# Kernel optimization log

Hardware: AMD Instinct MI355X
Metric: run time of the kernel (lower is better)

## Reference

```python
import jax, jax.numpy as jnp
import numpy as np

D_MODEL = 256
D_CLIP = 768
NHEAD = 8
HEAD_DIM = D_MODEL // NHEAD
Q_LEN = 100
B = 32
T_LEN = 1203


def setup_inputs() -> dict:
    key = jax.random.key(0)
    ks = jax.random.split(key, 16)
    xav = lambda k, o, i: jax.random.uniform(k, (o, i), jnp.float32, -1.0, 1.0) * np.sqrt(6.0 / (o + i))
    return {
        "tgt": jax.random.normal(ks[0], (Q_LEN, B, D_MODEL), jnp.float32),
        "text_classification": jax.random.normal(ks[1], (T_LEN, D_CLIP), jnp.float32),
        "query_pos": jax.random.normal(ks[2], (Q_LEN, B, D_MODEL), jnp.float32),
        "out_of_vocab_logits": jax.random.normal(ks[3], (B, Q_LEN, T_LEN), jnp.float32),
        "Wq": xav(ks[4], D_MODEL, D_MODEL), "bq": jnp.zeros((D_MODEL,), jnp.float32),
        "Wk": xav(ks[5], D_MODEL, D_CLIP), "bk": jnp.zeros((D_MODEL,), jnp.float32),
        "Wv": xav(ks[6], D_MODEL, D_CLIP), "bv": jnp.zeros((D_MODEL,), jnp.float32),
        "Wo": xav(ks[7], D_MODEL, D_MODEL), "bo": jnp.zeros((D_MODEL,), jnp.float32),
        "ln_g": jnp.ones((D_MODEL,), jnp.float32), "ln_b": jnp.zeros((D_MODEL,), jnp.float32),
        "logit_scale": jnp.asarray(np.log(1 / 0.07), jnp.float32),
    }


def _l2norm(x, eps=1e-6):
    # F.normalize: x / max(||x||, eps)
    n = jnp.sqrt(jnp.sum(x * x, axis=-1, keepdims=True))
    return x / jnp.maximum(n, eps)


def _layernorm(x, g, b, eps=1e-5):
    mu = jnp.mean(x, axis=-1, keepdims=True)
    var = jnp.mean((x - mu) ** 2, axis=-1, keepdims=True)
    return (x - mu) * jax.lax.rsqrt(var + eps) * g + b


def reference(tgt, text_classification, query_pos, out_of_vocab_logits,
              Wq, bq, Wk, bk, Wv, bv, Wo, bo, ln_g, ln_b, logit_scale):
    qin = tgt + query_pos                       # (Q, B, d_model)
    q = qin @ Wq.T + bq                         # (Q, B, d_model)
    # text embeddings shared across batch (2D path)
    k = text_classification @ Wk.T + bk         # (T, d_model)
    v = text_classification @ Wv.T + bv         # (T, d_model)

    q = q.transpose(1, 0, 2).reshape(B, Q_LEN, NHEAD, HEAD_DIM).transpose(0, 2, 1, 3)  # (B,h,Q,hd)
    k = k.reshape(T_LEN, NHEAD, HEAD_DIM).transpose(1, 0, 2)                            # (h,T,hd)
    v = v.reshape(T_LEN, NHEAD, HEAD_DIM).transpose(1, 0, 2)                            # (h,T,hd)

    q = _l2norm(q)
    k = _l2norm(k)
    scale = jnp.minimum(jnp.exp(logit_scale), 100.0)
    in_vocab = jnp.einsum('bhqd,hkd->bhqk', q, k) * scale                                # (B,h,Q,T)

    alpha = jnp.linspace(0.0, 1.0, NHEAD, dtype=in_vocab.dtype).reshape(1, NHEAD, 1, 1)
    logits = in_vocab * (1.0 - alpha) + out_of_vocab_logits[:, None] * alpha

    attn = jax.nn.softmax(logits, axis=-1)
    out = jnp.einsum('bhqk,hkd->bhqd', attn, v)                                          # (B,h,Q,hd)
    out = out.transpose(0, 2, 1, 3).reshape(B, Q_LEN, D_MODEL).transpose(1, 0, 2)        # (Q,B,d_model)
    out = out @ Wo.T + bo

    # forward_post: residual + layernorm (dropout=0)
    return _layernorm(tgt + out, ln_g, ln_b)
```

## Files before the change

kernel.cpp:

```cpp
#include <hip/hip_runtime.h>
#include <hip/hip_bf16.h>
#include <math.h>

#define D_MODEL 256
#define D_CLIP 768
#define NHEAD 8
#define HEAD_DIM 32
#define Q_LEN 100
#define BB 32
#define T_LEN 1203
#define TPAD 1216
#define MQ (Q_LEN*BB)
#define LOG2E 1.4426950408889634f

typedef __bf16 bf16_t;
typedef __bf16 bf16x8 __attribute__((ext_vector_type(8)));
typedef __bf16 bf16x4 __attribute__((ext_vector_type(4)));
typedef float f32x4 __attribute__((ext_vector_type(4)));

static __device__ __forceinline__ bf16_t to_bf16(float x) { return (bf16_t)x; }

__global__ void prep_kernel(const float* __restrict__ tgt, const float* __restrict__ qpos,
                            const float* __restrict__ text, const float* __restrict__ Wq,
                            const float* __restrict__ Wk, const float* __restrict__ Wv,
                            const float* __restrict__ Wo, const float* __restrict__ oov,
                            bf16_t* __restrict__ qin_bf, bf16_t* __restrict__ conv_dst,
                            float* __restrict__ oov_ws) {
    int idx = blockIdx.x * 256 + threadIdx.x;
    if (idx >= 1529248) return;
    if (idx < 204800) {
        float4 a = ((const float4*)tgt)[idx];
        float4 b = ((const float4*)qpos)[idx];
        bf16x4 r = { to_bf16(a.x + b.x), to_bf16(a.y + b.y),
                     to_bf16(a.z + b.z), to_bf16(a.w + b.w) };
        *(bf16x4*)(qin_bf + (size_t)idx * 4) = r;
    } else if (idx < 566848) {
        int j = idx - 204800;
        const float4* src;
        if (j < 230976)      src = (const float4*)text + j;
        else if (j < 247360) src = (const float4*)Wq + (j - 230976);
        else if (j < 296512) src = (const float4*)Wk + (j - 247360);
        else if (j < 345664) src = (const float4*)Wv + (j - 296512);
        else                 src = (const float4*)Wo + (j - 345664);
        float4 v = *src;
        bf16x4 r = { to_bf16(v.x), to_bf16(v.y), to_bf16(v.z), to_bf16(v.w) };
        *(bf16x4*)(conv_dst + (size_t)j * 4) = r;
    } else {
        int j = idx - 566848;
        ((float4*)oov_ws)[j] = ((const float4*)oov)[j];
    }
}

__launch_bounds__(256)
__global__ void proj_kernel(const bf16_t* __restrict__ qin_bf, const bf16_t* __restrict__ text_bf,
                            const bf16_t* __restrict__ wq, const bf16_t* __restrict__ wk,
                            const bf16_t* __restrict__ wv,
                            const float* __restrict__ bq, const float* __restrict__ bk,
                            const float* __restrict__ bv,
                            bf16_t* __restrict__ qn, bf16_t* __restrict__ kn,
                            bf16_t* __restrict__ vT) {
    const int bid = blockIdx.y;
    int z, xt;
    if (bid < 50)      { z = 0; xt = bid; }
    else if (bid < 69) { z = 1; xt = bid - 50; }
    else               { z = 2; xt = bid - 69; }
    const int j = blockIdx.x;
    const int nbase = j * 32;
    const int M = (z == 0) ? MQ : T_LEN;
    const int K = (z == 0) ? D_MODEL : D_CLIP;
    const bf16_t* W = (z == 0) ? wq : (z == 1 ? wk : wv);
    const float* bias = (z == 0) ? bq : (z == 1 ? bk : bv);

    const int wave = threadIdx.x >> 6;
    const int lane = threadIdx.x & 63;
    const int c16 = lane & 15;
    const int quad = lane >> 4;
    const int mbase = xt * 64 + wave * 16;

    f32x4 a0 = (f32x4){0.f, 0.f, 0.f, 0.f};
    f32x4 a1 = (f32x4){0.f, 0.f, 0.f, 0.f};

    const int arow = (mbase + c16 < M) ? (mbase + c16) : (M - 1);
    const bf16_t* Apb = ((z == 0) ? qin_bf : text_bf) + (size_t)arow * K + quad * 8;
    const bf16_t* W0 = W + (size_t)(nbase + c16) * K + quad * 8;
    const bf16_t* W1 = W + (size_t)(nbase + 16 + c16) * K + quad * 8;
    const int ksteps = K / 32;
    #pragma unroll 4
    for (int ks = 0; ks < ksteps; ks++) {
        bf16x8 af = *(const bf16x8*)(Apb + ks * 32);
        bf16x8 b0 = *(const bf16x8*)(W0 + ks * 32);
        bf16x8 b1 = *(const bf16x8*)(W1 + ks * 32);
        a0 = __builtin_amdgcn_mfma_f32_16x16x32_bf16(af, b0, a0, 0, 0, 0);
        a1 = __builtin_amdgcn_mfma_f32_16x16x32_bf16(af, b1, a1, 0, 0, 0);
    }

    float b0s = bias[nbase + c16];
    float b1s = bias[nbase + 16 + c16];
    #pragma unroll
    for (int r = 0; r < 4; r++) { a0[r] += b0s; a1[r] += b1s; }
    if (z < 2) {
        #pragma unroll
        for (int r = 0; r < 4; r++) {
            float s = a0[r] * a0[r] + a1[r] * a1[r];
            #pragma unroll
            for (int o = 1; o < 16; o <<= 1) s += __shfl_xor(s, o);
            float sc = 1.0f / fmaxf(sqrtf(s), 1e-6f);
            a0[r] *= sc; a1[r] *= sc;
        }
    }
    #pragma unroll
    for (int r = 0; r < 4; r++) {
        int m = mbase + quad * 4 + r;
        if (m >= M) continue;
        if (z == 0) {
            int q = m >> 5, b = m & 31;
            size_t base = ((size_t)(b * NHEAD + j) * Q_LEN + q) * HEAD_DIM;
            qn[base + c16] = to_bf16(a0[r]);
            qn[base + 16 + c16] = to_bf16(a1[r]);
        } else if (z == 1) {
            size_t base = ((size_t)j * T_LEN + m) * HEAD_DIM;
            kn[base + c16] = to_bf16(a0[r]);
            kn[base + 16 + c16] = to_bf16(a1[r]);
        } else {
            vT[(size_t)(j * 32 + c16) * TPAD + m] = to_bf16(a0[r]);
            vT[(size_t)(j * 32 + 16 + c16) * TPAD + m] = to_bf16(a1[r]);
        }
    }
}

__launch_bounds__(256)
__global__ void attn_kernel(const bf16_t* __restrict__ qn, const bf16_t* __restrict__ kn,
                            const bf16_t* __restrict__ vT, const float* __restrict__ oov,
                            const float* __restrict__ logit_scale,
                            bf16_t* __restrict__ attn_out) {
    const int qt = blockIdx.x;
    const int h = blockIdx.y;
    const int b = blockIdx.z;
    const int qbase = qt * 16;
    const int wave = threadIdx.x >> 6;
    const int lane = threadIdx.x & 63;
    const int c16 = lane & 15;
    const int quad = lane >> 4;

    __shared__ __align__(16) bf16_t p_lds[4][2][16][40];
    __shared__ float l_lds[4][16];
    __shared__ float o_lds[4][32][16];

    const float scl = fminf(expf(logit_scale[0]), 100.0f);
    const float alpha = (float)h * (1.0f / 7.0f);
    const float sscale = scl * (1.0f - alpha) * LOG2E;
    const float oscale = alpha * LOG2E;
    const float mfix = sscale + 20.0f * oscale;

    const int q = qbase + c16;
    const int qc = (q < Q_LEN) ? q : (Q_LEN - 1);
    bf16x8 qf = *(const bf16x8*)(qn + ((size_t)(b * NHEAD + h) * Q_LEN + qc) * HEAD_DIM + quad * 8);

    f32x4 olo = (f32x4){0.f, 0.f, 0.f, 0.f};
    f32x4 ohi = (f32x4){0.f, 0.f, 0.f, 0.f};
    float l_s = 0.0f;

    const bf16_t* knh = kn + (size_t)h * T_LEN * HEAD_DIM;
    const bf16_t* vTh = vT + (size_t)h * HEAD_DIM * TPAD;
    const float* oovr = oov + ((size_t)b * Q_LEN + qc) * T_LEN;
    const f32x4 zero = (f32x4){0.f, 0.f, 0.f, 0.f};

    bf16x8 kA0, kA1, kB0, kB1, vA0, vA1, vB0, vB1;
    float4 oA0, oA1, oB0, oB1;

    #define LOAD_PAIR(P, kA0_, kA1_, kB0_, kB1_, vA0_, vA1_, vB0_, vB1_, oA0_, oA1_, oB0_, oB1_) \
        { const int tb0_ = (P) * 64; const int tb1_ = tb0_ + 32;                                   \
          kA0_ = *(const bf16x8*)(knh + (size_t)(tb0_ + c16) * HEAD_DIM + quad * 8);               \
          kA1_ = *(const bf16x8*)(knh + (size_t)(tb0_ + 16 + c16) * HEAD_DIM + quad * 8);          \
          kB0_ = *(const bf16x8*)(knh + (size_t)(tb1_ + c16) * HEAD_DIM + quad * 8);               \
          kB1_ = *(const bf16x8*)(knh + (size_t)(tb1_ + 16 + c16) * HEAD_DIM + quad * 8);          \
          vA0_ = *(const bf16x8*)(vTh + (size_t)c16 * TPAD + tb0_ + quad * 8);                     \
          vA1_ = *(const bf16x8*)(vTh + (size_t)(16 + c16) * TPAD + tb0_ + quad * 8);              \
          vB0_ = *(const bf16x8*)(vTh + (size_t)c16 * TPAD + tb1_ + quad * 8);                     \
          vB1_ = *(const bf16x8*)(vTh + (size_t)(16 + c16) * TPAD + tb1_ + quad * 8);              \
          oA0_ = *(const float4*)(oovr + tb0_ + quad * 4);                                         \
          oA1_ = *(const float4*)(oovr + tb0_ + 16 + quad * 4);                                    \
          oB0_ = *(const float4*)(oovr + tb1_ + quad * 4);                                         \
          oB1_ = *(const float4*)(oovr + tb1_ + 16 + quad * 4); }

    if (wave < 18) LOAD_PAIR(wave, kA0, kA1, kB0, kB1, vA0, vA1, vB0, vB1, oA0, oA1, oB0, oB1);

    for (int p = wave; p < 18; p += 4) {
        const int pn = (p + 4 < 18) ? (p + 4) : 17;
        bf16x8 nkA0, nkA1, nkB0, nkB1, nvA0, nvA1, nvB0, nvB1;
        float4 noA0, noA1, noB0, noB1;
        LOAD_PAIR(pn, nkA0, nkA1, nkB0, nkB1, nvA0, nvA1, nvB0, nvB1, noA0, noA1, noB0, noB1);

        f32x4 s00 = __builtin_amdgcn_mfma_f32_16x16x32_bf16(kA0, qf, zero, 0, 0, 0);
        f32x4 s01 = __builtin_amdgcn_mfma_f32_16x16x32_bf16(kA1, qf, zero, 0, 0, 0);
        f32x4 s10 = __builtin_amdgcn_mfma_f32_16x16x32_bf16(kB0, qf, zero, 0, 0, 0);
        f32x4 s11 = __builtin_amdgcn_mfma_f32_16x16x32_bf16(kB1, qf, zero, 0, 0, 0);
        float pa0[4], pa1[4], pb0[4], pb1[4];
        float ovA0[4] = {oA0.x, oA0.y, oA0.z, oA0.w};
        float ovA1[4] = {oA1.x, oA1.y, oA1.z, oA1.w};
        float ovB0[4] = {oB0.x, oB0.y, oB0.z, oB0.w};
        float ovB1[4] = {oB1.x, oB1.y, oB1.z, oB1.w};
        #pragma unroll
        for (int r = 0; r < 4; r++) {
            pa0[r] = exp2f(fmaf(s00[r], sscale, fmaf(ovA0[r], oscale, -mfix)));
            pa1[r] = exp2f(fmaf(s01[r], sscale, fmaf(ovA1[r], oscale, -mfix)));
            pb0[r] = exp2f(fmaf(s10[r], sscale, fmaf(ovB0[r], oscale, -mfix)));
            pb1[r] = exp2f(fmaf(s11[r], sscale, fmaf(ovB1[r], oscale, -mfix)));
        }
        l_s += ((pa0[0] + pa0[1]) + (pa0[2] + pa0[3])) + ((pa1[0] + pa1[1]) + (pa1[2] + pa1[3]))
             + ((pb0[0] + pb0[1]) + (pb0[2] + pb0[3])) + ((pb1[0] + pb1[1]) + (pb1[2] + pb1[3]));
        bf16x4 wA0 = { to_bf16(pa0[0]), to_bf16(pa0[1]), to_bf16(pa0[2]), to_bf16(pa0[3]) };
        bf16x4 wA1 = { to_bf16(pa1[0]), to_bf16(pa1[1]), to_bf16(pa1[2]), to_bf16(pa1[3]) };
        bf16x4 wB0 = { to_bf16(pb0[0]), to_bf16(pb0[1]), to_bf16(pb0[2]), to_bf16(pb0[3]) };
        bf16x4 wB1 = { to_bf16(pb1[0]), to_bf16(pb1[1]), to_bf16(pb1[2]), to_bf16(pb1[3]) };
        *(bf16x4*)&p_lds[wave][0][c16][quad * 4] = wA0;
        *(bf16x4*)&p_lds[wave][0][c16][16 + quad * 4] = wA1;
        *(bf16x4*)&p_lds[wave][1][c16][quad * 4] = wB0;
        *(bf16x4*)&p_lds[wave][1][c16][16 + quad * 4] = wB1;
        bf16x8 pf0 = *(const bf16x8*)(&p_lds[wave][0][c16][quad * 8]);
        bf16x8 pf1 = *(const bf16x8*)(&p_lds[wave][1][c16][quad * 8]);
        olo = __builtin_amdgcn_mfma_f32_16x16x32_bf16(vA0, pf0, olo, 0, 0, 0);
        ohi = __builtin_amdgcn_mfma_f32_16x16x32_bf16(vA1, pf0, ohi, 0, 0, 0);
        olo = __builtin_amdgcn_mfma_f32_16x16x32_bf16(vB0, pf1, olo, 0, 0, 0);
        ohi = __builtin_amdgcn_mfma_f32_16x16x32_bf16(vB1, pf1, ohi, 0, 0, 0);

        kA0 = nkA0; kA1 = nkA1; kB0 = nkB0; kB1 = nkB1;
        vA0 = nvA0; vA1 = nvA1; vB0 = nvB0; vB1 = nvB1;
        oA0 = noA0; oA1 = noA1; oB0 = noB0; oB1 = noB1;
    }
    #undef LOAD_PAIR

    if (wave == 2) {
        const int tb = 1152;
        bf16x8 kf0 = *(const bf16x8*)(knh + (size_t)(tb + c16) * HEAD_DIM + quad * 8);
        bf16x8 kf1 = *(const bf16x8*)(knh + (size_t)(tb + 16 + c16) * HEAD_DIM + quad * 8);
        float4 oa = *(const float4*)(oovr + tb + quad * 4);
        float4 oc = *(const float4*)(oovr + tb + 16 + quad * 4);
        bf16x8 v0 = *(const bf16x8*)(vTh + (size_t)c16 * TPAD + tb + quad * 8);
        bf16x8 v1 = *(const bf16x8*)(vTh + (size_t)(16 + c16) * TPAD + tb + quad * 8);
        f32x4 s0 = __builtin_amdgcn_mfma_f32_16x16x32_bf16(kf0, qf, zero, 0, 0, 0);
        f32x4 s1 = __builtin_amdgcn_mfma_f32_16x16x32_bf16(kf1, qf, zero, 0, 0, 0);
        float ova[4] = {oa.x, oa.y, oa.z, oa.w};
        float ovc[4] = {oc.x, oc.y, oc.z, oc.w};
        float p0[4], p1[4];
        #pragma unroll
        for (int r = 0; r < 4; r++) {
            p0[r] = exp2f(fmaf(s0[r], sscale, fmaf(ova[r], oscale, -mfix)));
            p1[r] = exp2f(fmaf(s1[r], sscale, fmaf(ovc[r], oscale, -mfix)));
        }
        l_s += ((p0[0] + p0[1]) + (p0[2] + p0[3])) + ((p1[0] + p1[1]) + (p1[2] + p1[3]));
        bf16x4 w0 = { to_bf16(p0[0]), to_bf16(p0[1]), to_bf16(p0[2]), to_bf16(p0[3]) };
        bf16x4 w1 = { to_bf16(p1[0]), to_bf16(p1[1]), to_bf16(p1[2]), to_bf16(p1[3]) };
        *(bf16x4*)&p_lds[wave][0][c16][quad * 4] = w0;
        *(bf16x4*)&p_lds[wave][0][c16][16 + quad * 4] = w1;
        bf16x8 pf = *(const bf16x8*)(&p_lds[wave][0][c16][quad * 8]);
        olo = __builtin_amdgcn_mfma_f32_16x16x32_bf16(v0, pf, olo, 0, 0, 0);
        ohi = __builtin_amdgcn_mfma_f32_16x16x32_bf16(v1, pf, ohi, 0, 0, 0);
    }

    if (wave == 3) {
        const int tb = 1184;
        int t1c = tb + 16 + c16;
        if (t1c >= T_LEN) t1c = T_LEN - 1;
        bf16x8 kf0 = *(const bf16x8*)(knh + (size_t)(tb + c16) * HEAD_DIM + quad * 8);
        bf16x8 kf1 = *(const bf16x8*)(knh + (size_t)t1c * HEAD_DIM + quad * 8);
        bf16x8 v0 = *(const bf16x8*)(vTh + (size_t)c16 * TPAD + tb + quad * 8);
        bf16x8 v1 = *(const bf16x8*)(vTh + (size_t)(16 + c16) * TPAD + tb + quad * 8);
        f32x4 s0 = __builtin_amdgcn_mfma_f32_16x16x32_bf16(kf0, qf, zero, 0, 0, 0);
        f32x4 s1 = __builtin_amdgcn_mfma_f32_16x16x32_bf16(kf1, qf, zero, 0, 0, 0);
        float p0[4], p1[4];
        #pragma unroll
        for (int r = 0; r < 4; r++) {
            int ta = tb + quad * 4 + r;
            int tb2 = tb + 16 + quad * 4 + r;
            float ova = oovr[ta];
            p0[r] = exp2f(fmaf(s0[r], sscale, fmaf(ova, oscale, -mfix)));
            if (tb2 < T_LEN) {
                float ovc = oovr[tb2];
                p1[r] = exp2f(fmaf(s1[r], sscale, fmaf(ovc, oscale, -mfix)));
            } else {
                p1[r] = 0.0f;
            }
        }
        l_s += ((p0[0] + p0[1]) + (p0[2] + p0[3])) + ((p1[0] + p1[1]) + (p1[2] + p1[3]));
        bf16x4 w0 = { to_bf16(p0[0]), to_bf16(p0[1]), to_bf16(p0[2]), to_bf16(p0[3]) };
        bf16x4 w1 = { to_bf16(p1[0]), to_bf16(p1[1]), to_bf16(p1[2]), to_bf16(p1[3]) };
        *(bf16x4*)&p_lds[wave][0][c16][quad * 4] = w0;
        *(bf16x4*)&p_lds[wave][0][c16][16 + quad * 4] = w1;
        bf16x8 pf = *(const bf16x8*)(&p_lds[wave][0][c16][quad * 8]);
        olo = __builtin_amdgcn_mfma_f32_16x16x32_bf16(v0, pf, olo, 0, 0, 0);
        ohi = __builtin_amdgcn_mfma_f32_16x16x32_bf16(v1, pf, ohi, 0, 0, 0);
    }

    l_s += __shfl_xor(l_s, 16);
    l_s += __shfl_xor(l_s, 32);
    if (quad == 0) l_lds[wave][c16] = l_s;
    #pragma unroll
    for (int r = 0; r < 4; r++) {
        o_lds[wave][quad * 4 + r][c16] = olo[r];
        o_lds[wave][16 + quad * 4 + r][c16] = ohi[r];
    }
    __syncthreads();
    const int q16 = threadIdx.x & 15;
    const int dd = threadIdx.x >> 4;
    float L = l_lds[0][q16] + l_lds[1][q16] + l_lds[2][q16] + l_lds[3][q16];
    const float invL = 1.0f / L;
    const int qout = qbase + q16;
    if (qout < Q_LEN) {
        #pragma unroll
        for (int half = 0; half < 2; half++) {
            int d = half * 16 + dd;
            float O = o_lds[0][d][q16] + o_lds[1][d][q16] +
                      o_lds[2][d][q16] + o_lds[3][d][q16];
            attn_out[((size_t)qout * BB + b) * D_MODEL + h * HEAD_DIM + d] = to_bf16(O * invL);
        }
    }
}

__launch_bounds__(256)
__global__ void out_kernel(const bf16_t* __restrict__ attn, const bf16_t* __restrict__ wo,
                           const float* __restrict__ bo, const float* __restrict__ tgt,
                           const float* __restrict__ ln_g, const float* __restrict__ ln_b,
                           float* __restrict__ out) {
    const int xt = blockIdx.x;
    const int wave = threadIdx.x >> 6;
    const int lane = threadIdx.x & 63;
    const int c16 = lane & 15;
    const int quad = lane >> 4;
    const int mbase = xt * 16;

    __shared__ float xs[16][264];

    f32x4 acc[4];
    #pragma unroll
    for (int i = 0; i < 4; i++) acc[i] = (f32x4){0.f, 0.f, 0.f, 0.f};
    const bf16_t* Ap = attn + (size_t)(mbase + c16) * D_MODEL + quad * 8;
    #pragma unroll
    for (int ks = 0; ks < 8; ks++) {
        bf16x8 af = *(const bf16x8*)(Ap + ks * 32);
        #pragma unroll
        for (int nt = 0; nt < 4; nt++) {
            int n = wave * 64 + nt * 16 + c16;
            bf16x8 bfr = *(const bf16x8*)(wo + (size_t)n * D_MODEL + ks * 32 + quad * 8);
            acc[nt] = __builtin_amdgcn_mfma_f32_16x16x32_bf16(af, bfr, acc[nt], 0, 0, 0);
        }
    }
    #pragma unroll
    for (int nt = 0; nt < 4; nt++) {
        int col = wave * 64 + nt * 16 + c16;
        float bb_ = bo[col];
        #pragma unroll
        for (int r = 0; r < 4; r++) {
            int m = mbase + quad * 4 + r;
            xs[quad * 4 + r][col] = acc[nt][r] + bb_ + tgt[(size_t)m * D_MODEL + col];
        }
    }
    __syncthreads();
    const int row = threadIdx.x >> 4;
    const int seg = threadIdx.x & 15;
    float sx = 0.f, sxx = 0.f;
    #pragma unroll
    for (int i = 0; i < 16; i++) {
        float x = xs[row][seg * 16 + i];
        sx += x; sxx += x * x;
    }
    #pragma unroll
    for (int o = 1; o < 16; o <<= 1) { sx += __shfl_xor(sx, o); sxx += __shfl_xor(sxx, o); }
    float mu = sx * (1.0f / 256.0f);
    float var = sxx * (1.0f / 256.0f) - mu * mu;
    float rstd = rsqrtf(fmaxf(var, 0.0f) + 1e-5f);
    size_t obase = (size_t)(mbase + row) * D_MODEL;
    #pragma unroll
    for (int i = 0; i < 16; i++) {
        int cidx = seg * 16 + i;
        out[obase + cidx] = (xs[row][cidx] - mu) * rstd * ln_g[cidx] + ln_b[cidx];
    }
}

extern "C" void kernel_launch(void* const* d_in, const int* in_sizes, int n_in,
                              void* d_out, int out_size, void* d_ws, size_t ws_size,
                              hipStream_t stream) {
    const float* tgt  = (const float*)d_in[0];
    const float* text = (const float*)d_in[1];
    const float* qpos = (const float*)d_in[2];
    const float* oov  = (const float*)d_in[3];
    const float* Wq = (const float*)d_in[4];
    const float* bq = (const float*)d_in[5];
    const float* Wk = (const float*)d_in[6];
    const float* bk = (const float*)d_in[7];
    const float* Wv = (const float*)d_in[8];
    const float* bv = (const float*)d_in[9];
    const float* Wo = (const float*)d_in[10];
    const float* bo = (const float*)d_in[11];
    const float* ln_g = (const float*)d_in[12];
    const float* ln_b = (const float*)d_in[13];
    const float* lsc  = (const float*)d_in[14];

    bf16_t* wsb = (bf16_t*)d_ws;
    bf16_t* text_bf = wsb + 0;
    bf16_t* wq_bf   = wsb + 923904;
    bf16_t* wk_bf   = wsb + 989440;
    bf16_t* wv_bf   = wsb + 1186048;
    bf16_t* wo_bf   = wsb + 1382656;
    bf16_t* qin_bf  = wsb + 1448192;
    bf16_t* qn      = wsb + 2267392;
    bf16_t* kn      = wsb + 3086592;
    bf16_t* vT      = wsb + 3394560;
    bf16_t* attn    = wsb + 3705856;
    float* oov_ws   = (float*)((char*)d_ws + 9050112);
    float* out      = (float*)d_out;

    prep_kernel<<<5975, 256, 0, stream>>>(tgt, qpos, text, Wq, Wk, Wv, Wo, oov,
                                          qin_bf, text_bf, oov_ws);
    proj_kernel<<<dim3(8, 88, 1), 256, 0, stream>>>(qin_bf, text_bf, wq_bf, wk_bf, wv_bf,
                                                    bq, bk, bv, qn, kn, vT);
    attn_kernel<<<dim3(7, 8, 32), 256, 0, stream>>>(qn, kn, vT, oov_ws, lsc, attn);
    out_kernel<<<200, 256, 0, stream>>>(attn, wo_bf, bo, tgt, ln_g, ln_b, out);
}
```

Before: 172.8 us.

## Stage per-head K in LDS and drop redundant oov copy in prep

Result: faster. 158.6 us (-8.2%).

```diff
diff --git a/kernel.cpp b/kernel.cpp
--- a/kernel.cpp
+++ b/kernel.cpp
@@ -23,18 +23,18 @@
 __global__ void prep_kernel(const float* __restrict__ tgt, const float* __restrict__ qpos,
                             const float* __restrict__ text, const float* __restrict__ Wq,
                             const float* __restrict__ Wk, const float* __restrict__ Wv,
-                            const float* __restrict__ Wo, const float* __restrict__ oov,
-                            bf16_t* __restrict__ qin_bf, bf16_t* __restrict__ conv_dst,
-                            float* __restrict__ oov_ws) {
+                            const float* __restrict__ Wo,
+                            bf16_t* __restrict__ qin_bf, bf16_t* __restrict__ conv_dst) {
     int idx = blockIdx.x * 256 + threadIdx.x;
-    if (idx >= 1529248) return;
+    if (idx >= 566848) return;
+    float4 v;
+    bf16_t* dst;
     if (idx < 204800) {
         float4 a = ((const float4*)tgt)[idx];
         float4 b = ((const float4*)qpos)[idx];
-        bf16x4 r = { to_bf16(a.x + b.x), to_bf16(a.y + b.y),
-                     to_bf16(a.z + b.z), to_bf16(a.w + b.w) };
-        *(bf16x4*)(qin_bf + (size_t)idx * 4) = r;
-    } else if (idx < 566848) {
+        v = make_float4(a.x + b.x, a.y + b.y, a.z + b.z, a.w + b.w);
+        dst = qin_bf + idx * 4;
+    } else {
         int j = idx - 204800;
         const float4* src;
         if (j < 230976)      src = (const float4*)text + j;
@@ -42,13 +42,11 @@
         else if (j < 296512) src = (const float4*)Wk + (j - 247360);
         else if (j < 345664) src = (const float4*)Wv + (j - 296512);
         else                 src = (const float4*)Wo + (j - 345664);
-        float4 v = *src;
-        bf16x4 r = { to_bf16(v.x), to_bf16(v.y), to_bf16(v.z), to_bf16(v.w) };
-        *(bf16x4*)(conv_dst + (size_t)j * 4) = r;
-    } else {
-        int j = idx - 566848;
-        ((float4*)oov_ws)[j] = ((const float4*)oov)[j];
-    }
+        v = *src;
+        dst = conv_dst + (size_t)j * 4;
+    }
+    bf16x4 r = { to_bf16(v.x), to_bf16(v.y), to_bf16(v.z), to_bf16(v.w) };
+    *(bf16x4*)dst = r;
 }
 
 __launch_bounds__(256)
@@ -128,23 +126,24 @@
     }
 }
 
-__launch_bounds__(256)
+__launch_bounds__(896)
 __global__ void attn_kernel(const bf16_t* __restrict__ qn, const bf16_t* __restrict__ kn,
                             const bf16_t* __restrict__ vT, const float* __restrict__ oov,
                             const float* __restrict__ logit_scale,
                             bf16_t* __restrict__ attn_out) {
-    const int qt = blockIdx.x;
+    const int b = blockIdx.x;
     const int h = blockIdx.y;
-    const int b = blockIdx.z;
-    const int qbase = qt * 16;
-    const int wave = threadIdx.x >> 6;
-    const int lane = threadIdx.x & 63;
+    const int tid = threadIdx.x;
+    const int w = tid >> 6;
+    const int lane = tid & 63;
     const int c16 = lane & 15;
     const int quad = lane >> 4;
-
-    __shared__ __align__(16) bf16_t p_lds[4][2][16][40];
-    __shared__ float l_lds[4][16];
-    __shared__ float o_lds[4][32][16];
+    const int qt = w >> 1;
+    const int thalf = w & 1;
+    const int qbase = qt * 16;
+
+    __shared__ __align__(16) unsigned int k_lds[24320];
+    __shared__ __align__(16) bf16_t p_lds[14][2][16][40];
 
     const float scl = fminf(expf(logit_scale[0]), 100.0f);
     const float alpha = (float)h * (1.0f / 7.0f);
@@ -152,49 +151,54 @@
     const float oscale = alpha * LOG2E;
     const float mfix = sscale + 20.0f * oscale;
 
-    const int q = qbase + c16;
-    const int qc = (q < Q_LEN) ? q : (Q_LEN - 1);
+    const bf16_t* knh = kn + (size_t)h * T_LEN * HEAD_DIM;
+    const bf16_t* vTh = vT + (size_t)h * HEAD_DIM * TPAD;
+
+    const int qc = (qbase + c16 < Q_LEN) ? (qbase + c16) : (Q_LEN - 1);
     bf16x8 qf = *(const bf16x8*)(qn + ((size_t)(b * NHEAD + h) * Q_LEN + qc) * HEAD_DIM + quad * 8);
+    const float* oovr = oov + ((size_t)b * Q_LEN + qc) * T_LEN;
+    const f32x4 zero = (f32x4){0.f, 0.f, 0.f, 0.f};
+
+    {
+        const unsigned int* knw = (const unsigned int*)knh;
+        for (int idx = tid; idx < 19248; idx += 896)
+            k_lds[(idx >> 4) * 20 + (idx & 15)] = knw[idx];
+    }
 
     f32x4 olo = (f32x4){0.f, 0.f, 0.f, 0.f};
     f32x4 ohi = (f32x4){0.f, 0.f, 0.f, 0.f};
     float l_s = 0.0f;
 
-    const bf16_t* knh = kn + (size_t)h * T_LEN * HEAD_DIM;
-    const bf16_t* vTh = vT + (size_t)h * HEAD_DIM * TPAD;
-    const float* oovr = oov + ((size_t)b * Q_LEN + qc) * T_LEN;
-    const f32x4 zero = (f32x4){0.f, 0.f, 0.f, 0.f};
-
-    bf16x8 kA0, kA1, kB0, kB1, vA0, vA1, vB0, vB1;
+    #define KFRAG(trow) (*(const bf16x8*)&k_lds[(unsigned)(trow) * 20 + quad * 4])
+    #define LOADPV(P, vA0_, vA1_, vB0_, vB1_, oA0_, oA1_, oB0_, oB1_)                   \
+        { const int tb0_ = (P) * 64; const int tb1_ = tb0_ + 32;                         \
+          vA0_ = *(const bf16x8*)(vTh + (size_t)c16 * TPAD + tb0_ + quad * 8);           \
+          vA1_ = *(const bf16x8*)(vTh + (size_t)(16 + c16) * TPAD + tb0_ + quad * 8);    \
+          vB0_ = *(const bf16x8*)(vTh + (size_t)c16 * TPAD + tb1_ + quad * 8);           \
+          vB1_ = *(const bf16x8*)(vTh + (size_t)(16 + c16) * TPAD + tb1_ + quad * 8);    \
+          oA0_ = *(const float4*)(oovr + tb0_ + quad * 4);                               \
+          oA1_ = *(const float4*)(oovr + tb0_ + 16 + quad * 4);                          \
+          oB0_ = *(const float4*)(oovr + tb1_ + quad * 4);                               \
+          oB1_ = *(const float4*)(oovr + tb1_ + 16 + quad * 4); }
+
+    bf16x8 vA0, vA1, vB0, vB1;
     float4 oA0, oA1, oB0, oB1;
-
-    #define LOAD_PAIR(P, kA0_, kA1_, kB0_, kB1_, vA0_, vA1_, vB0_, vB1_, oA0_, oA1_, oB0_, oB1_) \
-        { const int tb0_ = (P) * 64; const int tb1_ = tb0_ + 32;                                   \
-          kA0_ = *(const bf16x8*)(knh + (size_t)(tb0_ + c16) * HEAD_DIM + quad * 8);               \
-          kA1_ = *(const bf16x8*)(knh + (size_t)(tb0_ + 16 + c16) * HEAD_DIM + quad * 8);          \
-          kB0_ = *(const bf16x8*)(knh + (size_t)(tb1_ + c16) * HEAD_DIM + quad * 8);               \
-          kB1_ = *(const bf16x8*)(knh + (size_t)(tb1_ + 16 + c16) * HEAD_DIM + quad * 8);          \
-          vA0_ = *(const bf16x8*)(vTh + (size_t)c16 * TPAD + tb0_ + quad * 8);                     \
-          vA1_ = *(const bf16x8*)(vTh + (size_t)(16 + c16) * TPAD + tb0_ + quad * 8);              \
-          vB0_ = *(const bf16x8*)(vTh + (size_t)c16 * TPAD + tb1_ + quad * 8);                     \
-          vB1_ = *(const bf16x8*)(vTh + (size_t)(16 + c16) * TPAD + tb1_ + quad * 8);              \
-          oA0_ = *(const float4*)(oovr + tb0_ + quad * 4);                                         \
-          oA1_ = *(const float4*)(oovr + tb0_ + 16 + quad * 4);                                    \
-          oB0_ = *(const float4*)(oovr + tb1_ + quad * 4);                                         \
-          oB1_ = *(const float4*)(oovr + tb1_ + 16 + quad * 4); }
-
-    if (wave < 18) LOAD_PAIR(wave, kA0, kA1, kB0, kB1, vA0, vA1, vB0, vB1, oA0, oA1, oB0, oB1);
-
-    for (int p = wave; p < 18; p += 4) {
-        const int pn = (p + 4 < 18) ? (p + 4) : 17;
-        bf16x8 nkA0, nkA1, nkB0, nkB1, nvA0, nvA1, nvB0, nvB1;
+    LOADPV(thalf, vA0, vA1, vB0, vB1, oA0, oA1, oB0, oB1);
+
+    __syncthreads();
+
+    for (int p = thalf; p < 18; p += 2) {
+        const int pn = (p + 2 < 18) ? (p + 2) : p;
+        bf16x8 nvA0, nvA1, nvB0, nvB1;
         float4 noA0, noA1, noB0, noB1;
-        LOAD_PAIR(pn, nkA0, nkA1, nkB0, nkB1, nvA0, nvA1, nvB0, nvB1, noA0, noA1, noB0, noB1);
-
-        f32x4 s00 = __builtin_amdgcn_mfma_f32_16x16x32_bf16(kA0, qf, zero, 0, 0, 0);
-        f32x4 s01 = __builtin_amdgcn_mfma_f32_16x16x32_bf16(kA1, qf, zero, 0, 0, 0);
-        f32x4 s10 = __builtin_amdgcn_mfma_f32_16x16x32_bf16(kB0, qf, zero, 0, 0, 0);
-        f32x4 s11 = __builtin_amdgcn_mfma_f32_16x16x32_bf16(kB1, qf, zero, 0, 0, 0);
+        LOADPV(pn, nvA0, nvA1, nvB0, nvB1, noA0, noA1, noB0, noB1);
+
+        const int tb0 = p * 64, tb1 = tb0 + 32;
+        f32x4 s00 = __builtin_amdgcn_mfma_f32_16x16x32_bf16(KFRAG(tb0 + c16), qf, zero, 0, 0, 0);
+        f32x4 s01 = __builtin_amdgcn_mfma_f32_16x16x32_bf16(KFRAG(tb0 + 16 + c16), qf, zero, 0, 0, 0);
+        f32x4 s10 = __builtin_amdgcn_mfma_f32_16x16x32_bf16(KFRAG(tb1 + c16), qf, zero, 0, 0, 0);
+        f32x4 s11 = __builtin_amdgcn_mfma_f32_16x16x32_bf16(KFRAG(tb1 + 16 + c16), qf, zero, 0, 0, 0);
+
         float pa0[4], pa1[4], pb0[4], pb1[4];
         float ovA0[4] = {oA0.x, oA0.y, oA0.z, oA0.w};
         float ovA1[4] = {oA1.x, oA1.y, oA1.z, oA1.w};
@@ -213,106 +217,108 @@
         bf16x4 wA1 = { to_bf16(pa1[0]), to_bf16(pa1[1]), to_bf16(pa1[2]), to_bf16(pa1[3]) };
         bf16x4 wB0 = { to_bf16(pb0[0]), to_bf16(pb0[1]), to_bf16(pb0[2]), to_bf16(pb0[3]) };
         bf16x4 wB1 = { to_bf16(pb1[0]), to_bf16(pb1[1]), to_bf16(pb1[2]), to_bf16(pb1[3]) };
-        *(bf16x4*)&p_lds[wave][0][c16][quad * 4] = wA0;
-        *(bf16x4*)&p_lds[wave][0][c16][16 + quad * 4] = wA1;
-        *(bf16x4*)&p_lds[wave][1][c16][quad * 4] = wB0;
-        *(bf16x4*)&p_lds[wave][1][c16][16 + quad * 4] = wB1;
-        bf16x8 pf0 = *(const bf16x8*)(&p_lds[wave][0][c16][quad * 8]);
-        bf16x8 pf1 = *(const bf16x8*)(&p_lds[wave][1][c16][quad * 8]);
+        *(bf16x4*)&p_lds[w][0][c16][quad * 4] = wA0;
+        *(bf16x4*)&p_lds[w][0][c16][16 + quad * 4] = wA1;
+        *(bf16x4*)&p_lds[w][1][c16][quad * 4] = wB0;
+        *(bf16x4*)&p_lds[w][1][c16][16 + quad * 4] = wB1;
+        bf16x8 pf0 = *(const bf16x8*)(&p_lds[w][0][c16][quad * 8]);
+        bf16x8 pf1 = *(const bf16x8*)(&p_lds[w][1][c16][quad * 8]);
         olo = __builtin_amdgcn_mfma_f32_16x16x32_bf16(vA0, pf0, olo, 0, 0, 0);
         ohi = __builtin_amdgcn_mfma_f32_16x16x32_bf16(vA1, pf0, ohi, 0, 0, 0);
         olo = __builtin_amdgcn_mfma_f32_16x16x32_bf16(vB0, pf1, olo, 0, 0, 0);
         ohi = __builtin_amdgcn_mfma_f32_16x16x32_bf16(vB1, pf1, ohi, 0, 0, 0);
 
-        kA0 = nkA0; kA1 = nkA1; kB0 = nkB0; kB1 = nkB1;
         vA0 = nvA0; vA1 = nvA1; vB0 = nvB0; vB1 = nvB1;
         oA0 = noA0; oA1 = noA1; oB0 = noB0; oB1 = noB1;
     }
-    #undef LOAD_PAIR
-
-    if (wave == 2) {
-        const int tb = 1152;
-        bf16x8 kf0 = *(const bf16x8*)(knh + (size_t)(tb + c16) * HEAD_DIM + quad * 8);
-        bf16x8 kf1 = *(const bf16x8*)(knh + (size_t)(tb + 16 + c16) * HEAD_DIM + quad * 8);
-        float4 oa = *(const float4*)(oovr + tb + quad * 4);
-        float4 oc = *(const float4*)(oovr + tb + 16 + quad * 4);
-        bf16x8 v0 = *(const bf16x8*)(vTh + (size_t)c16 * TPAD + tb + quad * 8);
-        bf16x8 v1 = *(const bf16x8*)(vTh + (size_t)(16 + c16) * TPAD + tb + quad * 8);
-        f32x4 s0 = __builtin_amdgcn_mfma_f32_16x16x32_bf16(kf0, qf, zero, 0, 0, 0);
-        f32x4 s1 = __builtin_amdgcn_mfma_f32_16x16x32_bf16(kf1, qf, zero, 0, 0, 0);
-        float ova[4] = {oa.x, oa.y, oa.z, oa.w};
-        float ovc[4] = {oc.x, oc.y, oc.z, oc.w};
-        float p0[4], p1[4];
-        #pragma unroll
-        for (int r = 0; r < 4; r++) {
-            p0[r] = exp2f(fmaf(s0[r], sscale, fmaf(ova[r], oscale, -mfix)));
-            p1[r] = exp2f(fmaf(s1[r], sscale, fmaf(ovc[r], oscale, -mfix)));
-        }
-        l_s += ((p0[0] + p0[1]) + (p0[2] + p0[3])) + ((p1[0] + p1[1]) + (p1[2] + p1[3]));
-        bf16x4 w0 = { to_bf16(p0[0]), to_bf16(p0[1]), to_bf16(p0[2]), to_bf16(p0[3]) };
-        bf16x4 w1 = { to_bf16(p1[0]), to_bf16(p1[1]), to_bf16(p1[2]), to_bf16(p1[3]) };
-        *(bf16x4*)&p_lds[wave][0][c16][quad * 4] = w0;
-        *(bf16x4*)&p_lds[wave][0][c16][16 + quad * 4] = w1;
-        bf16x8 pf = *(const bf16x8*)(&p_lds[wave][0][c16][quad * 8]);
-        olo = __builtin_amdgcn_mfma_f32_16x16x32_bf16(v0, pf, olo, 0, 0, 0);
-        ohi = __builtin_amdgcn_mfma_f32_16x16x32_bf16(v1, pf, ohi, 0, 0, 0);
-    }
-
-    if (wave == 3) {
-        const int tb = 1184;
-        int t1c = tb + 16 + c16;
-        if (t1c >= T_LEN) t1c = T_LEN - 1;
-        bf16x8 kf0 = *(const bf16x8*)(knh + (size_t)(tb + c16) * HEAD_DIM + quad * 8);
-        bf16x8 kf1 = *(const bf16x8*)(knh + (size_t)t1c * HEAD_DIM + quad * 8);
-        bf16x8 v0 = *(const bf16x8*)(vTh + (size_t)c16 * TPAD + tb + quad * 8);
-        bf16x8 v1 = *(const bf16x8*)(vTh + (size_t)(16 + c16) * TPAD + tb + quad * 8);
-        f32x4 s0 = __builtin_amdgcn_mfma_f32_16x16x32_bf16(kf0, qf, zero, 0, 0, 0);
-        f32x4 s1 = __builtin_amdgcn_mfma_f32_16x16x32_bf16(kf1, qf, zero, 0, 0, 0);
-        float p0[4], p1[4];
-        #pragma unroll
-        for (int r = 0; r < 4; r++) {
-            int ta = tb + quad * 4 + r;
-            int tb2 = tb + 16 + quad * 4 + r;
-            float ova = oovr[ta];
-            p0[r] = exp2f(fmaf(s0[r], sscale, fmaf(ova, oscale, -mfix)));
-            if (tb2 < T_LEN) {
-                float ovc = oovr[tb2];
-                p1[r] = exp2f(fmaf(s1[r], sscale, fmaf(ovc, oscale, -mfix)));
-            } else {
-                p1[r] = 0.0f;
+
+    if (thalf == 0) {
+        {
+            const int tb = 1152;
+            f32x4 s0 = __builtin_amdgcn_mfma_f32_16x16x32_bf16(KFRAG(tb + c16), qf, zero, 0, 0, 0);
+            f32x4 s1 = __builtin_amdgcn_mfma_f32_16x16x32_bf16(KFRAG(tb + 16 + c16), qf, zero, 0, 0, 0);
+            float4 oa = *(const float4*)(oovr + tb + quad * 4);
+            float4 oc = *(const float4*)(oovr + tb + 16 + quad * 4);
+            bf16x8 v0 = *(const bf16x8*)(vTh + (size_t)c16 * TPAD + tb + quad * 8);
+            bf16x8 v1 = *(const bf16x8*)(vTh + (size_t)(16 + c16) * TPAD + tb + quad * 8);
+            float ova[4] = {oa.x, oa.y, oa.z, oa.w};
+            float ovc[4] = {oc.x, oc.y, oc.z, oc.w};
+            float p0[4], p1[4];
+            #pragma unroll
+            for (int r = 0; r < 4; r++) {
+                p0[r] = exp2f(fmaf(s0[r], sscale, fmaf(ova[r], oscale, -mfix)));
+                p1[r] = exp2f(fmaf(s1[r], sscale, fmaf(ovc[r], oscale, -mfix)));
             }
-        }
-        l_s += ((p0[0] + p0[1]) + (p0[2] + p0[3])) + ((p1[0] + p1[1]) + (p1[2] + p1[3]));
-        bf16x4 w0 = { to_bf16(p0[0]), to_bf16(p0[1]), to_bf16(p0[2]), to_bf16(p0[3]) };
-        bf16x4 w1 = { to_bf16(p1[0]), to_bf16(p1[1]), to_bf16(p1[2]), to_bf16(p1[3]) };
-        *(bf16x4*)&p_lds[wave][0][c16][quad * 4] = w0;
-        *(bf16x4*)&p_lds[wave][0][c16][16 + quad * 4] = w1;
-        bf16x8 pf = *(const bf16x8*)(&p_lds[wave][0][c16][quad * 8]);
-        olo = __builtin_amdgcn_mfma_f32_16x16x32_bf16(v0, pf, olo, 0, 0, 0);
-        ohi = __builtin_amdgcn_mfma_f32_16x16x32_bf16(v1, pf, ohi, 0, 0, 0);
-    }
+            l_s += ((p0[0] + p0[1]) + (p0[2] + p0[3])) + ((p1[0] + p1[1]) + (p1[2] + p1[3]));
+            bf16x4 w0 = { to_bf16(p0[0]), to_bf16(p0[1]), to_bf16(p0[2]), to_bf16(p0[3]) };
+            bf16x4 w1 = { to_bf16(p1[0]), to_bf16(p1[1]), to_bf16(p1[2]), to_bf16(p1[3]) };
+            *(bf16x4*)&p_lds[w][0][c16][quad * 4] = w0;
+            *(bf16x4*)&p_lds[w][0][c16][16 + quad * 4] = w1;
+            bf16x8 pf = *(const bf16x8*)(&p_lds[w][0][c16][quad * 8]);
+            olo = __builtin_amdgcn_mfma_f32_16x16x32_bf16(v0, pf, olo, 0, 0, 0);
+            ohi = __builtin_amdgcn_mfma_f32_16x16x32_bf16(v1, pf, ohi, 0, 0, 0);
+        }
+        {
+            const int tb = 1184;
+            int tr1 = tb + 16 + c16;
+            if (tr1 > T_LEN - 1) tr1 = T_LEN - 1;
+            f32x4 s0 = __builtin_amdgcn_mfma_f32_16x16x32_bf16(KFRAG(tb + c16), qf, zero, 0, 0, 0);
+            f32x4 s1 = __builtin_amdgcn_mfma_f32_16x16x32_bf16(KFRAG(tr1), qf, zero, 0, 0, 0);
+            float4 oa = *(const float4*)(oovr + tb + quad * 4);
+            bf16x8 v0 = *(const bf16x8*)(vTh + (size_t)c16 * TPAD + tb + quad * 8);
+            bf16x8 v1 = *(const bf16x8*)(vTh + (size_t)(16 + c16) * TPAD + tb + quad * 8);
+            float ova[4] = {oa.x, oa.y, oa.z, oa.w};
+            float p0[4], p1[4];
+            #pragma unroll
+            for (int r = 0; r < 4; r++) {
+                p0[r] = exp2f(fmaf(s0[r], sscale, fmaf(ova[r], oscale, -mfix)));
+                int t2 = tb + 16 + quad * 4 + r;
+                if (t2 < T_LEN) {
+                    float ovc = oovr[t2];
+                    p1[r] = exp2f(fmaf(s1[r], sscale, fmaf(ovc, oscale, -mfix)));
+                } else {
+                    p1[r] = 0.0f;
+                }
+            }
+            l_s += ((p0[0] + p0[1]) + (p0[2] + p0[3])) + ((p1[0] + p1[1]) + (p1[2] + p1[3]));
+            bf16x4 w0 = { to_bf16(p0[0]), to_bf16(p0[1]), to_bf16(p0[2]), to_bf16(p0[3]) };
+            bf16x4 w1 = { to_bf16(p1[0]), to_bf16(p1[1]), to_bf16(p1[2]), to_bf16(p1[3]) };
+            *(bf16x4*)&p_lds[w][1][c16][quad * 4] = w0;
+            *(bf16x4*)&p_lds[w][1][c16][16 + quad * 4] = w1;
+            bf16x8 pf = *(const bf16x8*)(&p_lds[w][1][c16][quad * 8]);
+            olo = __builtin_amdgcn_mfma_f32_16x16x32_bf16(v0, pf, olo, 0, 0, 0);
+            ohi = __builtin_amdgcn_mfma_f32_16x16x32_bf16(v1, pf, ohi, 0, 0, 0);
+        }
+    }
+    #undef KFRAG
+    #undef LOADPV
 
     l_s += __shfl_xor(l_s, 16);
     l_s += __shfl_xor(l_s, 32);
-    if (quad == 0) l_lds[wave][c16] = l_s;
+
+    __syncthreads();
+    float* mrg = (float*)k_lds;
+    const int mb = (thalf * 7 + qt) * 528;
+    if (quad == 0) mrg[mb + c16] = l_s;
     #pragma unroll
     for (int r = 0; r < 4; r++) {
-        o_lds[wave][quad * 4 + r][c16] = olo[r];
-        o_lds[wave][16 + quad * 4 + r][c16] = ohi[r];
+        mrg[mb + 16 + (quad * 4 + r) * 16 + c16] = olo[r];
+        mrg[mb + 16 + (16 + quad * 4 + r) * 16 + c16] = ohi[r];
     }
     __syncthreads();
-    const int q16 = threadIdx.x & 15;
-    const int dd = threadIdx.x >> 4;
-    float L = l_lds[0][q16] + l_lds[1][q16] + l_lds[2][q16] + l_lds[3][q16];
-    const float invL = 1.0f / L;
-    const int qout = qbase + q16;
-    if (qout < Q_LEN) {
+    if (thalf == 0) {
+        const int d = lane & 31;
+        const int qg = lane >> 5;
+        const int b0 = qt * 528, b1 = (7 + qt) * 528;
         #pragma unroll
-        for (int half = 0; half < 2; half++) {
-            int d = half * 16 + dd;
-            float O = o_lds[0][d][q16] + o_lds[1][d][q16] +
-                      o_lds[2][d][q16] + o_lds[3][d][q16];
-            attn_out[((size_t)qout * BB + b) * D_MODEL + h * HEAD_DIM + d] = to_bf16(O * invL);
+        for (int jj = 0; jj < 8; jj++) {
+            int q16 = qg * 8 + jj;
+            int qo = qbase + q16;
+            if (qo < Q_LEN) {
+                float L = mrg[b0 + q16] + mrg[b1 + q16];
+                float O = mrg[b0 + 16 + d * 16 + q16] + mrg[b1 + 16 + d * 16 + q16];
+                attn_out[((size_t)qo * BB + b) * D_MODEL + h * HEAD_DIM + d] = to_bf16(O / L);
+            }
         }
     }
 }
@@ -407,13 +413,11 @@
     bf16_t* kn      = wsb + 3086592;
     bf16_t* vT      = wsb + 3394560;
     bf16_t* attn    = wsb + 3705856;
-    float* oov_ws   = (float*)((char*)d_ws + 9050112);
     float* out      = (float*)d_out;
 
-    prep_kernel<<<5975, 256, 0, stream>>>(tgt, qpos, text, Wq, Wk, Wv, Wo, oov,
-                                          qin_bf, text_bf, oov_ws);
+    prep_kernel<<<2215, 256, 0, stream>>>(tgt, qpos, text, Wq, Wk, Wv, Wo, qin_bf, text_bf);
     proj_kernel<<<dim3(8, 88, 1), 256, 0, stream>>>(qin_bf, text_bf, wq_bf, wk_bf, wv_bf,
                                                     bq, bk, bv, qn, kn, vT);
-    attn_kernel<<<dim3(7, 8, 32), 256, 0, stream>>>(qn, kn, vT, oov_ws, lsc, attn);
+    attn_kernel<<<dim3(32, 8), 896, 0, stream>>>(qn, kn, vT, oov, lsc, attn);
     out_kernel<<<200, 256, 0, stream>>>(attn, wo_bf, bo, tgt, ln_g, ln_b, out);
 }
```
